# Kernel tuning notes

Hardware: AMD Instinct MI355X
Metric: run time of the kernel (lower is better)

The kernel has to match this reference:

```python
import jax, jax.numpy as jnp
import numpy as np

N = 4096          # nodes (single graph, batch=None)
E = 65536         # edges (avg degree 16)
C = 256           # hidden_channels
L = 3             # num_layers
H = 8             # attention heads
EPS = 1e-5        # batchnorm eps


def setup_inputs() -> dict:
    key = jax.random.key(0)
    ks = iter(jax.random.split(key, 64))
    s = 0.05
    d = {}
    d['x'] = jax.random.normal(next(ks), (N, 1), dtype=jnp.float32)
    d['edge_index'] = jax.random.randint(next(ks), (2, E), 0, N, dtype=jnp.int32)
    # input projection Linear(1, C)
    d['lin1_w'] = jax.random.normal(next(ks), (C, 1), dtype=jnp.float32) * s
    d['lin1_b'] = jnp.zeros((C,), dtype=jnp.float32)
    # GIN MLP: Linear(C,C) -> ReLU -> Linear(C,C), stacked over layers
    d['gin_w1'] = jax.random.normal(next(ks), (L, C, C), dtype=jnp.float32) * s
    d['gin_b1'] = jnp.zeros((L, C), dtype=jnp.float32)
    d['gin_w2'] = jax.random.normal(next(ks), (L, C, C), dtype=jnp.float32) * s
    d['gin_b2'] = jnp.zeros((L, C), dtype=jnp.float32)
    # MultiheadAttention projections
    for nm in ['attn_wq', 'attn_wk', 'attn_wv', 'attn_wo']:
        d[nm] = jax.random.normal(next(ks), (L, C, C), dtype=jnp.float32) * s
    for nm in ['attn_bq', 'attn_bk', 'attn_bv', 'attn_bo']:
        d[nm] = jnp.zeros((L, C), dtype=jnp.float32)
    # three BatchNorms per GPSConv layer
    for nm in ['bn1', 'bn2', 'bn3']:
        d[nm + '_g'] = jnp.ones((L, C), dtype=jnp.float32)
        d[nm + '_b'] = jnp.zeros((L, C), dtype=jnp.float32)
    # GPSConv feedforward: Linear(C, 2C) -> ReLU -> Linear(2C, C)
    d['mlp_w1'] = jax.random.normal(next(ks), (L, 2 * C, C), dtype=jnp.float32) * s
    d['mlp_b1'] = jnp.zeros((L, 2 * C), dtype=jnp.float32)
    d['mlp_w2'] = jax.random.normal(next(ks), (L, C, 2 * C), dtype=jnp.float32) * s
    d['mlp_b2'] = jnp.zeros((L, C), dtype=jnp.float32)
    return d


def _bn(v, g, b):
    # training-mode BatchNorm1d over the node dimension (biased variance)
    m = v.mean(0)
    var = v.var(0)
    return (v - m) * jax.lax.rsqrt(var + EPS) * g + b


def _gps_forward(x, edge_index, lin1_w, lin1_b, gin_w1, gin_b1, gin_w2, gin_b2,
                 attn_wq, attn_bq, attn_wk, attn_bk, attn_wv, attn_bv,
                 attn_wo, attn_bo, bn1_g, bn1_b, bn2_g, bn2_b, bn3_g, bn3_b,
                 mlp_w1, mlp_b1, mlp_w2, mlp_b2):
    h = x @ lin1_w.T + lin1_b                     # [N, C]
    src, dst = edge_index[0], edge_index[1]
    dh = C // H
    scale = 1.0 / jnp.sqrt(jnp.float32(dh))
    for l in range(L):
        xin = h
        # --- GIN branch: gather -> scatter-sum -> MLP ---
        agg = jax.ops.segment_sum(xin[src], dst, num_segments=N)   # [N, C]
        z = xin + agg                                               # eps=0
        z = jax.nn.relu(z @ gin_w1[l].T + gin_b1[l]) @ gin_w2[l].T + gin_b2[l]
        h1 = _bn(z + xin, bn1_g[l], bn1_b[l])
        # --- global multihead attention over all N nodes ---
        q = (xin @ attn_wq[l].T + attn_bq[l]).reshape(N, H, dh)
        k = (xin @ attn_wk[l].T + attn_bk[l]).reshape(N, H, dh)
        v = (xin @ attn_wv[l].T + attn_bv[l]).reshape(N, H, dh)
        scores = jnp.einsum('nhd,mhd->hnm', q, k) * scale           # [H, N, N]
        a = jax.nn.softmax(scores, axis=-1)
        o = jnp.einsum('hnm,mhd->nhd', a, v).reshape(N, C)
        o = o @ attn_wo[l].T + attn_bo[l]
        h2 = _bn(o + xin, bn2_g[l], bn2_b[l])
        # --- combine + feedforward ---
        s = h1 + h2
        m = jax.nn.relu(s @ mlp_w1[l].T + mlp_b1[l]) @ mlp_w2[l].T + mlp_b2[l]
        h = _bn(s + m, bn3_g[l], bn3_b[l])
    return h


def reference(x, edge_index, lin1_w, lin1_b, gin_w1, gin_b1, gin_w2, gin_b2,
              attn_wq, attn_bq, attn_wk, attn_bk, attn_wv, attn_bv,
              attn_wo, attn_bo, bn1_g, bn1_b, bn2_g, bn2_b, bn3_g, bn3_b,
              mlp_w1, mlp_b1, mlp_w2, mlp_b2):
    return _gps_forward(x, edge_index, lin1_w, lin1_b, gin_w1, gin_b1, gin_w2,
                        gin_b2, attn_wq, attn_bq, attn_wk, attn_bk, attn_wv,
                        attn_bv, attn_wo, attn_bo, bn1_g, bn1_b, bn2_g, bn2_b,
                        bn3_g, bn3_b, mlp_w1, mlp_b1, mlp_w2, mlp_b2)
```

## Files before the change

### kernel.cpp

```cpp
#include <hip/hip_runtime.h>

#define NN 4096
#define NE 65536
#define C 256
#define NL 3
#define NH 8
#define DH 32
#define EPS 1e-5f
#define SPLIT 2
#define KT8 (NN/128/SPLIT)
#define ATTN_BLKS ((NN/128)*NH*SPLIT)
#define VS 136

typedef __bf16 bf16x8 __attribute__((ext_vector_type(8)));
typedef __bf16 bf16x4v __attribute__((ext_vector_type(4)));
typedef float f32x4 __attribute__((ext_vector_type(4)));
typedef short bf16x4s __attribute__((ext_vector_type(4)));

#define QSCALE (0.17677669529663687f * 1.4426950408889634f)

#define CC1 (C*C)
#define GS 72

__global__ __launch_bounds__(256) void prep_w(const float* __restrict__ s0,
        const float* __restrict__ s1, const float* __restrict__ s2,
        const float* __restrict__ s3, const float* __restrict__ s4,
        const float* __restrict__ s5, const float* __restrict__ s6,
        const float* __restrict__ s7, __bf16* __restrict__ dst) {
    int g = blockIdx.y;
    int i = (blockIdx.x*256 + threadIdx.x)*4;
    const float* src; int n;
    switch (g) {
        case 0: src=s0; n=3*CC1; break;
        case 1: src=s1; n=3*CC1; break;
        case 2: src=s2; n=3*CC1; break;
        case 3: src=s3; n=3*CC1; break;
        case 4: src=s4; n=3*CC1; break;
        case 5: src=s5; n=3*CC1; break;
        case 6: src=s6; n=6*CC1; break;
        default: src=s7; n=6*CC1; break;
    }
    if (i >= n) return;
    size_t off;
    if (g >= 2 && g <= 4) {
        int l = i >> 16, rem = i & (CC1-1);
        off = (size_t)(6 + 3*l + (g-2))*CC1 + rem;
    } else {
        size_t base = (g==0) ? 0 : (g==1) ? 3*(size_t)CC1 : (g==5) ? 15*(size_t)CC1
                    : (g==6) ? 18*(size_t)CC1 : 24*(size_t)CC1;
        off = base + i;
    }
    float4 t = *(const float4*)(src + i);
    bf16x4v o = {(__bf16)t.x, (__bf16)t.y, (__bf16)t.z, (__bf16)t.w};
    *(bf16x4v*)(dst + off) = o;
}

__global__ __launch_bounds__(256) void lin1_kernel(const float* __restrict__ x,
        const float* __restrict__ w, const float* __restrict__ b,
        __bf16* __restrict__ out) {
    int n = blockIdx.x, c = threadIdx.x;
    out[(size_t)n*C + c] = (__bf16)(x[n]*w[c] + b[c]);
}

__global__ __launch_bounds__(256) void hist_kernel(const int* __restrict__ ei,
        int* __restrict__ cnt) {
    int e = blockIdx.x*256 + threadIdx.x;
    atomicAdd(&cnt[ei[NE + e]], 1);
}

__global__ __launch_bounds__(256) void scan_kernel(const int* __restrict__ cnt,
        int* __restrict__ rowptr, int* __restrict__ cursor) {
    __shared__ int tot[256];
    __shared__ int pre[257];
    int t = threadIdx.x;
    int base = t*16;
    int local[16];
    int s = 0;
    #pragma unroll
    for (int i = 0; i < 16; i++) { local[i] = s; s += cnt[base+i]; }
    tot[t] = s;
    __syncthreads();
    if (t == 0) {
        int acc = 0;
        for (int i = 0; i < 256; i++) { pre[i] = acc; acc += tot[i]; }
        pre[256] = acc;
    }
    __syncthreads();
    int off = pre[t];
    #pragma unroll
    for (int i = 0; i < 16; i++) {
        rowptr[base+i] = off + local[i];
        cursor[base+i] = off + local[i];
    }
    if (t == 0) rowptr[NN] = pre[256];
}

__global__ __launch_bounds__(256) void fill_kernel(const int* __restrict__ ei,
        int* __restrict__ cursor, int* __restrict__ eidsrc) {
    int e = blockIdx.x*256 + threadIdx.x;
    int dst = ei[NE + e], src = ei[e];
    int pos = atomicAdd(&cursor[dst], 1);
    eidsrc[pos] = src;
}

template<int QKV, int BN, int COMB>
__device__ __forceinline__ void gemm_core(int bm, int bn,
        const __bf16* A, const float* A2f, const __bf16* A2b, const __bf16* W,
        const float* b0, const float* b1, const float* b2,
        const __bf16* add1, const __bf16* add2,
        __bf16* out, __bf16* vt, __bf16* ktp, float* stats,
        const float* coefs,
        const float* st1, const float* g1, const float* bb1,
        const float* st2, const float* g2, const float* bb2,
        const float* lsum,
        int K, int Nout, int relu, __bf16* As, __bf16* Ws) {
    int tid = threadIdx.x;
    int wave = tid >> 6, lane = tid & 63;
    int ln = lane & 15, quad = lane >> 4;
    int row = tid >> 2, kseg = (tid & 3) * 16;
    f32x4 acc[4] = {};
    for (int k0 = 0; k0 < K; k0 += 64) {
        __syncthreads();
        {
            bf16x8 a0, a1;
            if constexpr (COMB) {
                int rowg = bm + row;
                int head = (k0 + kseg) >> 5;
                float w[SPLIT];
                float tot = 0.f;
                #pragma unroll
                for (int zz = 0; zz < SPLIT; zz++) {
                    w[zz] = lsum[((size_t)zz*NH + head)*NN + rowg];
                    tot += w[zz];
                }
                float inv = 1.0f / tot;
                float v[16] = {};
                #pragma unroll
                for (int zz = 0; zz < SPLIT; zz++) {
                    const __bf16* p = &A[((size_t)zz*NN + rowg)*C + k0 + kseg];
                    bf16x8 x0 = *(const bf16x8*)p, x1 = *(const bf16x8*)(p + 8);
                    #pragma unroll
                    for (int j = 0; j < 8; j++) {
                        v[j]   += w[zz]*(float)x0[j];
                        v[8+j] += w[zz]*(float)x1[j];
                    }
                }
                #pragma unroll
                for (int j = 0; j < 8; j++) {
                    a0[j] = (__bf16)(v[j]*inv);
                    a1[j] = (__bf16)(v[8+j]*inv);
                }
            } else {
                const __bf16* ap = &A[(size_t)(bm+row)*K + k0 + kseg];
                a0 = *(const bf16x8*)ap;
                a1 = *(const bf16x8*)(ap + 8);
                if constexpr (BN == 1) {
                    const __bf16* p = &A2b[(size_t)(bm+row)*K + k0 + kseg];
                    bf16x8 z0 = *(const bf16x8*)p;
                    bf16x8 z1v = *(const bf16x8*)(p + 8);
                    float sc1[16], sh1[16], sc2[16], sh2[16];
                    #pragma unroll
                    for (int i = 0; i < 4; i++) {
                        *(float4*)&sc1[i*4] = *(const float4*)&coefs[k0 + kseg + i*4];
                        *(float4*)&sh1[i*4] = *(const float4*)&coefs[C + k0 + kseg + i*4];
                        *(float4*)&sc2[i*4] = *(const float4*)&coefs[2*C + k0 + kseg + i*4];
                        *(float4*)&sh2[i*4] = *(const float4*)&coefs[3*C + k0 + kseg + i*4];
                    }
                    #pragma unroll
                    for (int j = 0; j < 8; j++) {
                        a0[j] = (__bf16)((float)a0[j]*sc1[j] + sh1[j]
                                       + (float)z0[j]*sc2[j] + sh2[j]);
                        a1[j] = (__bf16)((float)a1[j]*sc1[8+j] + sh1[8+j]
                                       + (float)z1v[j]*sc2[8+j] + sh2[8+j]);
                    }
                } else if (A2f) {
                    const float* p = &A2f[(size_t)(bm+row)*K + k0 + kseg];
                    float4 t0 = *(const float4*)p;
                    float4 t1 = *(const float4*)(p+4);
                    float4 t2 = *(const float4*)(p+8);
                    float4 t3 = *(const float4*)(p+12);
                    a0[0]=(__bf16)((float)a0[0]+t0.x); a0[1]=(__bf16)((float)a0[1]+t0.y);
                    a0[2]=(__bf16)((float)a0[2]+t0.z); a0[3]=(__bf16)((float)a0[3]+t0.w);
                    a0[4]=(__bf16)((float)a0[4]+t1.x); a0[5]=(__bf16)((float)a0[5]+t1.y);
                    a0[6]=(__bf16)((float)a0[6]+t1.z); a0[7]=(__bf16)((float)a0[7]+t1.w);
                    a1[0]=(__bf16)((float)a1[0]+t2.x); a1[1]=(__bf16)((float)a1[1]+t2.y);
                    a1[2]=(__bf16)((float)a1[2]+t2.z); a1[3]=(__bf16)((float)a1[3]+t2.w);
                    a1[4]=(__bf16)((float)a1[4]+t3.x); a1[5]=(__bf16)((float)a1[5]+t3.y);
                    a1[6]=(__bf16)((float)a1[6]+t3.z); a1[7]=(__bf16)((float)a1[7]+t3.w);
                }
            }
            *(bf16x8*)&As[row*GS + kseg]     = a0;
            *(bf16x8*)&As[row*GS + kseg + 8] = a1;
            const __bf16* wp = &W[(size_t)(bn+row)*K + k0 + kseg];
            *(bf16x8*)&Ws[row*GS + kseg]     = *(const bf16x8*)wp;
            *(bf16x8*)&Ws[row*GS + kseg + 8] = *(const bf16x8*)(wp + 8);
        }
        __syncthreads();
        #pragma unroll
        for (int kt2 = 0; kt2 < 2; kt2++) {
            bf16x8 bfr = *(const bf16x8*)&Ws[(wave*16+ln)*GS + kt2*32 + quad*8];
            #pragma unroll
            for (int i = 0; i < 4; i++) {
                bf16x8 afr = *(const bf16x8*)&As[(i*16+ln)*GS + kt2*32 + quad*8];
                acc[i] = __builtin_amdgcn_mfma_f32_16x16x32_bf16(afr, bfr, acc[i], 0, 0, 0);
            }
        }
    }
    int col = bn + wave*16 + ln;
    if constexpr (QKV) {
        float bsv = col < 256 ? b0[col] : (col < 512 ? b1[col-256] : b2[col-512]);
        if (col < 256) {
            #pragma unroll
            for (int i = 0; i < 4; i++)
                #pragma unroll
                for (int rr = 0; rr < 4; rr++)
                    out[(size_t)(bm + i*16 + quad*4 + rr)*C + col] =
                        (__bf16)((acc[i][rr] + bsv) * (float)QSCALE);
        } else if (col < 512) {
            int hd = (col-256) >> 5, dh = (col-256) & 31;
            #pragma unroll
            for (int i = 0; i < 4; i++)
                #pragma unroll
                for (int rr = 0; rr < 4; rr++)
                    ktp[((size_t)hd*NN + bm + i*16 + quad*4 + rr)*DH + dh] =
                        (__bf16)(acc[i][rr] + bsv);
        } else {
            int vrow = col - 512;
            #pragma unroll
            for (int i = 0; i < 4; i++) {
                bf16x4v pk = {(__bf16)(acc[i][0]+bsv), (__bf16)(acc[i][1]+bsv),
                              (__bf16)(acc[i][2]+bsv), (__bf16)(acc[i][3]+bsv)};
                *(bf16x4v*)&vt[(size_t)vrow*NN + bm + i*16 + quad*4] = pk;
            }
        }
        return;
    }
    float bsv = b0[col];
    float sc1 = 0.f, sh1 = 0.f, sc2 = 0.f, sh2 = 0.f;
    if constexpr (BN == 2) {
        float m1 = st1[col]*(1.f/NN);
        sc1 = rsqrtf(st1[C+col]*(1.f/NN) - m1*m1 + EPS) * g1[col];
        sh1 = bb1[col] - m1*sc1;
        float m2 = st2[col]*(1.f/NN);
        sc2 = rsqrtf(st2[C+col]*(1.f/NN) - m2*m2 + EPS) * g2[col];
        sh2 = bb2[col] - m2*sc2;
    }
    float ssum = 0.f, ssq = 0.f;
    #pragma unroll
    for (int i = 0; i < 4; i++) {
        #pragma unroll
        for (int rr = 0; rr < 4; rr++) {
            int rw = bm + i*16 + quad*4 + rr;
            float vv = acc[i][rr] + bsv;
            if (relu) vv = fmaxf(vv, 0.f);
            size_t idx = (size_t)rw*Nout + col;
            if constexpr (BN == 2) {
                vv += (float)add1[idx]*sc1 + sh1 + (float)add2[idx]*sc2 + sh2;
            } else {
                if (add1) vv += (float)add1[idx];
                if (add2) vv += (float)add2[idx];
            }
            out[idx] = (__bf16)vv;
            ssum += vv; ssq += vv*vv;
        }
    }
    if (stats) {
        ssum += __shfl_xor(ssum, 16); ssum += __shfl_xor(ssum, 32);
        ssq  += __shfl_xor(ssq, 16);  ssq  += __shfl_xor(ssq, 32);
        if (quad == 0) {
            atomicAdd(&stats[col], ssum);
            atomicAdd(&stats[Nout + col], ssq);
        }
    }
}

__device__ __forceinline__ void attn_body(int t, const __bf16* __restrict__ qbuf,
        const __bf16* __restrict__ kt, const __bf16* __restrict__ vt,
        __bf16* __restrict__ opart, float* __restrict__ lsum, __bf16* lds) {
    int head = t & 7, z = t >> 8, qi = (t >> 3) & 31, qb = qi * 128;
    int hb = head * DH;
    int tid = threadIdx.x;
    int wave = tid >> 6, lane = tid & 63;
    int ln = lane & 15, quad = lane >> 4;
    __bf16* Kb0 = lds;
    __bf16* Kb1 = lds + 4608;
    __bf16* Vb0 = lds + 9216;
    __bf16* Vb1 = lds + 9216 + 32*VS;

    bf16x8 qf[2];
    #pragma unroll
    for (int g = 0; g < 2; g++)
        qf[g] = *(const bf16x8*)&qbuf[(size_t)(qb + wave*32 + g*16 + ln)*C + hb + quad*8];

    f32x4 ot[2][2] = {};
    f32x4 la[2] = {};
    const bf16x4s ones = {(short)0x3F80, (short)0x3F80, (short)0x3F80, (short)0x3F80};
    const f32x4 zz = {0.f,0.f,0.f,0.f};

    int srow = tid >> 1, sseg = (tid & 1) * 16;
    int vd = tid >> 3, vseg = (tid & 7) * 16;
    int kt0 = z * KT8;
    const __bf16* kbase = &kt[(size_t)head*NN*DH];
    {
        int i0 = qi & (KT8-1);
        const __bf16* kp = &kbase[(size_t)((kt0+i0)*128 + srow)*DH + sseg];
        *(bf16x8*)&Kb0[srow*36 + sseg]     = *(const bf16x8*)kp;
        *(bf16x8*)&Kb0[srow*36 + sseg + 8] = *(const bf16x8*)(kp + 8);
        const __bf16* vp = &vt[(size_t)(hb + vd)*NN + (kt0+i0)*128 + vseg];
        *(bf16x8*)&Vb0[vd*VS + vseg]     = *(const bf16x8*)vp;
        *(bf16x8*)&Vb0[vd*VS + vseg + 8] = *(const bf16x8*)(vp + 8);
    }
    for (int ii = 0; ii < KT8; ii++) {
        int inext = (ii + 1 + qi) & (KT8-1);
        __bf16* Kc = (ii & 1) ? Kb1 : Kb0;
        __bf16* Kn = (ii & 1) ? Kb0 : Kb1;
        __bf16* Vc = (ii & 1) ? Vb1 : Vb0;
        __bf16* Vn = (ii & 1) ? Vb0 : Vb1;
        __syncthreads();
        bf16x8 nk0, nk1, nv0, nv1;
        bool hasNext = (ii + 1 < KT8);
        if (hasNext) {
            const __bf16* kp = &kbase[(size_t)((kt0+inext)*128 + srow)*DH + sseg];
            nk0 = *(const bf16x8*)kp;
            nk1 = *(const bf16x8*)(kp + 8);
            const __bf16* vp = &vt[(size_t)(hb + vd)*NN + (kt0+inext)*128 + vseg];
            nv0 = *(const bf16x8*)vp;
            nv1 = *(const bf16x8*)(vp + 8);
        }
        bf16x8 kfr[2][2];
        bf16x4s vfr[2][2][2];
        f32x4 stq[2][4];
        kfr[0][0] = *(const bf16x8*)&Kc[((0*16)+ln)*36 + quad*8];
        kfr[0][1] = *(const bf16x8*)&Kc[((1*16)+ln)*36 + quad*8];
        stq[0][0] = __builtin_amdgcn_mfma_f32_16x16x32_bf16(kfr[0][0], qf[0], zz, 0, 0, 0);
        stq[0][1] = __builtin_amdgcn_mfma_f32_16x16x32_bf16(kfr[0][0], qf[1], zz, 0, 0, 0);
        stq[0][2] = __builtin_amdgcn_mfma_f32_16x16x32_bf16(kfr[0][1], qf[0], zz, 0, 0, 0);
        stq[0][3] = __builtin_amdgcn_mfma_f32_16x16x32_bf16(kfr[0][1], qf[1], zz, 0, 0, 0);
        kfr[1][0] = *(const bf16x8*)&Kc[((2*16)+ln)*36 + quad*8];
        kfr[1][1] = *(const bf16x8*)&Kc[((3*16)+ln)*36 + quad*8];
        #pragma unroll
        for (int s = 0; s < 2; s++)
            #pragma unroll
            for (int h = 0; h < 2; h++)
                vfr[0][s][h] = *(const bf16x4s*)&Vc[(h*16+ln)*VS + s*16 + quad*4];
        #pragma unroll
        for (int pr = 0; pr < 4; pr++) {
            const int cur = pr & 1, nxt = cur ^ 1;
            if (pr < 2) {
                kfr[cur][0] = *(const bf16x8*)&Kc[(((pr+2)*2+0)*16+ln)*36 + quad*8];
                kfr[cur][1] = *(const bf16x8*)&Kc[(((pr+2)*2+1)*16+ln)*36 + quad*8];
            }
            if (pr < 3) {
                #pragma unroll
                for (int s = 0; s < 2; s++)
                    #pragma unroll
                    for (int h = 0; h < 2; h++)
                        vfr[nxt][s][h] = *(const bf16x4s*)&Vc[(h*16+ln)*VS + ((pr+1)*2+s)*16 + quad*4];
            }
            if (pr < 3) {
                __builtin_amdgcn_s_setprio(1);
                stq[nxt][0] = __builtin_amdgcn_mfma_f32_16x16x32_bf16(kfr[nxt][0], qf[0], zz, 0, 0, 0);
                stq[nxt][1] = __builtin_amdgcn_mfma_f32_16x16x32_bf16(kfr[nxt][0], qf[1], zz, 0, 0, 0);
                stq[nxt][2] = __builtin_amdgcn_mfma_f32_16x16x32_bf16(kfr[nxt][1], qf[0], zz, 0, 0, 0);
                stq[nxt][3] = __builtin_amdgcn_mfma_f32_16x16x32_bf16(kfr[nxt][1], qf[1], zz, 0, 0, 0);
                __builtin_amdgcn_s_setprio(0);
            }
            union { __bf16 b[4]; bf16x4s s; } pf00, pf01, pf10, pf11;
            #pragma unroll
            for (int rr = 0; rr < 4; rr++) {
                pf00.b[rr] = (__bf16)__builtin_amdgcn_exp2f(stq[cur][0][rr]);
                pf10.b[rr] = (__bf16)__builtin_amdgcn_exp2f(stq[cur][1][rr]);
                pf01.b[rr] = (__bf16)__builtin_amdgcn_exp2f(stq[cur][2][rr]);
                pf11.b[rr] = (__bf16)__builtin_amdgcn_exp2f(stq[cur][3][rr]);
            }
            __builtin_amdgcn_s_setprio(1);
            ot[0][0] = __builtin_amdgcn_mfma_f32_16x16x16bf16_1k(vfr[cur][0][0], pf00.s, ot[0][0], 0, 0, 0);
            ot[0][1] = __builtin_amdgcn_mfma_f32_16x16x16bf16_1k(vfr[cur][0][1], pf00.s, ot[0][1], 0, 0, 0);
            ot[1][0] = __builtin_amdgcn_mfma_f32_16x16x16bf16_1k(vfr[cur][0][0], pf10.s, ot[1][0], 0, 0, 0);
            ot[1][1] = __builtin_amdgcn_mfma_f32_16x16x16bf16_1k(vfr[cur][0][1], pf10.s, ot[1][1], 0, 0, 0);
            la[0]    = __builtin_amdgcn_mfma_f32_16x16x16bf16_1k(ones, pf00.s, la[0], 0, 0, 0);
            la[1]    = __builtin_amdgcn_mfma_f32_16x16x16bf16_1k(ones, pf10.s, la[1], 0, 0, 0);
            ot[0][0] = __builtin_amdgcn_mfma_f32_16x16x16bf16_1k(vfr[cur][1][0], pf01.s, ot[0][0], 0, 0, 0);
            ot[0][1] = __builtin_amdgcn_mfma_f32_16x16x16bf16_1k(vfr[cur][1][1], pf01.s, ot[0][1], 0, 0, 0);
            ot[1][0] = __builtin_amdgcn_mfma_f32_16x16x16bf16_1k(vfr[cur][1][0], pf11.s, ot[1][0], 0, 0, 0);
            ot[1][1] = __builtin_amdgcn_mfma_f32_16x16x16bf16_1k(vfr[cur][1][1], pf11.s, ot[1][1], 0, 0, 0);
            la[0]    = __builtin_amdgcn_mfma_f32_16x16x16bf16_1k(ones, pf01.s, la[0], 0, 0, 0);
            la[1]    = __builtin_amdgcn_mfma_f32_16x16x16bf16_1k(ones, pf11.s, la[1], 0, 0, 0);
            __builtin_amdgcn_s_setprio(0);
        }
        if (hasNext) {
            *(bf16x8*)&Kn[srow*36 + sseg]     = nk0;
            *(bf16x8*)&Kn[srow*36 + sseg + 8] = nk1;
            *(bf16x8*)&Vn[vd*VS + vseg]     = nv0;
            *(bf16x8*)&Vn[vd*VS + vseg + 8] = nv1;
        }
    }
    #pragma unroll
    for (int g = 0; g < 2; g++) {
        float l_ = la[g][0];
        float inv = 1.0f / l_;
        int qrow = qb + wave*32 + g*16 + ln;
        #pragma unroll
        for (int h = 0; h < 2; h++) {
            bf16x4v pk = {(__bf16)(ot[g][h][0]*inv), (__bf16)(ot[g][h][1]*inv),
                          (__bf16)(ot[g][h][2]*inv), (__bf16)(ot[g][h][3]*inv)};
            *(bf16x4v*)&opart[((size_t)z*NN + qrow)*C + hb + h*16 + quad*4] = pk;
        }
        if (quad == 0)
            lsum[((size_t)z*NH + head)*NN + qrow] = l_;
    }
}

__global__ __launch_bounds__(256) void qkv_agg_kernel(const __bf16* __restrict__ Hb,
        const __bf16* __restrict__ Wqkv, const float* __restrict__ bq,
        const float* __restrict__ bk, const float* __restrict__ bv,
        __bf16* __restrict__ qout, __bf16* __restrict__ ktout,
        __bf16* __restrict__ vtout,
        const int* __restrict__ rowptr, const int* __restrict__ eidsrc,
        float* __restrict__ agg) {
    __shared__ __bf16 lds[9216];
    int bx = blockIdx.x;
    if (bx < 768) {
        gemm_core<1,0,0>((bx & 63)*64, (bx >> 6)*64, Hb, nullptr, nullptr, Wqkv,
                bq, bk, bv, nullptr, nullptr, qout, vtout, ktout, nullptr,
                nullptr, nullptr, nullptr, nullptr, nullptr, nullptr, nullptr,
                nullptr, C, 768, 0, lds, lds + 4608);
        return;
    }
    int tid = threadIdx.x;
    int wave = tid >> 6, lane = tid & 63;
    int node = (bx - 768)*4 + wave;
    int beg = rowptr[node], end = rowptr[node+1];
    float s0 = 0.f, s1 = 0.f, s2 = 0.f, s3 = 0.f;
    for (int e = beg; e < end; e++) {
        int src = eidsrc[e];
        bf16x4v hv = *(const bf16x4v*)&Hb[(size_t)src*C + lane*4];
        s0 += (float)hv[0]; s1 += (float)hv[1];
        s2 += (float)hv[2]; s3 += (float)hv[3];
    }
    float4 o = {s0, s1, s2, s3};
    *(float4*)&agg[(size_t)node*C + lane*4] = o;
}

__global__ __launch_bounds__(256, 2) void gin1_attn_kernel(const __bf16* __restrict__ Hb,
        const float* __restrict__ agg, const __bf16* __restrict__ gw1,
        const float* __restrict__ gb1, __bf16* __restrict__ t1,
        const __bf16* __restrict__ qbuf, const __bf16* __restrict__ kt,
        const __bf16* __restrict__ vt,
        __bf16* __restrict__ opart, float* __restrict__ lsum) {
    __shared__ __bf16 lds[17920];
    int bx = blockIdx.x;
    if (bx < 256) {
        gemm_core<0,0,0>((bx >> 2)*64, (bx & 3)*64, Hb, agg, nullptr, gw1,
                gb1, nullptr, nullptr, nullptr, nullptr, t1, nullptr, nullptr,
                nullptr, nullptr, nullptr, nullptr, nullptr, nullptr, nullptr,
                nullptr, nullptr, C, C, 1, lds, lds + 4608);
        return;
    }
    attn_body(bx - 256, qbuf, kt, vt, opart, lsum, lds);
}

__global__ __launch_bounds__(256) void gin2_proj_kernel(const __bf16* __restrict__ t1,
        const __bf16* __restrict__ gw2, const float* __restrict__ gb2,
        const __bf16* __restrict__ Hb, __bf16* __restrict__ z1, float* __restrict__ st1,
        const __bf16* __restrict__ opart, const float* __restrict__ lsum,
        const __bf16* __restrict__ wop, const float* __restrict__ lbo,
        __bf16* __restrict__ z2, float* __restrict__ st2) {
    __shared__ __bf16 lds[9216];
    int bx = blockIdx.x;
    if (bx < 256) {
        gemm_core<0,0,0>((bx >> 2)*64, (bx & 3)*64, t1, nullptr, nullptr, gw2,
                gb2, nullptr, nullptr, Hb, nullptr, z1, nullptr, nullptr, st1,
                nullptr, nullptr, nullptr, nullptr, nullptr, nullptr, nullptr,
                nullptr, C, C, 0, lds, lds + 4608);
        return;
    }
    int t = bx - 256;
    gemm_core<0,0,1>((t >> 2)*64, (t & 3)*64, opart, nullptr, nullptr, wop,
            lbo, nullptr, nullptr, Hb, nullptr, z2, nullptr, nullptr, st2,
            nullptr, nullptr, nullptr, nullptr, nullptr, nullptr, nullptr,
            lsum, C, C, 0, lds, lds + 4608);
}

__global__ __launch_bounds__(256) void ff1_kernel(const __bf16* __restrict__ z1,
        const __bf16* __restrict__ z2, const __bf16* __restrict__ mw1,
        const float* __restrict__ lmb1, __bf16* __restrict__ hidden,
        const float* __restrict__ st1, const float* __restrict__ g1,
        const float* __restrict__ bb1, const float* __restrict__ st2,
        const float* __restrict__ g2, const float* __restrict__ bb2) {
    __shared__ __bf16 lds[9216];
    __shared__ float coefs[4*C];
    int tid = threadIdx.x;
    {
        float m = st1[tid]*(1.f/NN);
        float var = st1[C+tid]*(1.f/NN) - m*m;
        float s = rsqrtf(var + EPS) * g1[tid];
        coefs[tid] = s; coefs[C+tid] = bb1[tid] - m*s;
        m = st2[tid]*(1.f/NN);
        var = st2[C+tid]*(1.f/NN) - m*m;
        s = rsqrtf(var + EPS) * g2[tid];
        coefs[2*C+tid] = s; coefs[3*C+tid] = bb2[tid] - m*s;
    }
    int bx = blockIdx.x;
    gemm_core<0,1,0>((bx >> 3)*64, (bx & 7)*64, z1, nullptr, z2, mw1,
            lmb1, nullptr, nullptr, nullptr, nullptr, hidden, nullptr, nullptr,
            nullptr, coefs, nullptr, nullptr, nullptr, nullptr, nullptr, nullptr,
            nullptr, C, 2*C, 1, lds, lds + 4608);
}

__global__ __launch_bounds__(256) void ff2_kernel(const __bf16* __restrict__ hidden,
        const __bf16* __restrict__ mw2, const float* __restrict__ lmb2,
        const __bf16* __restrict__ z1, const __bf16* __restrict__ z2,
        __bf16* __restrict__ zbuf3, float* __restrict__ st3,
        const float* __restrict__ st1, const float* __restrict__ g1,
        const float* __restrict__ bb1, const float* __restrict__ st2,
        const float* __restrict__ g2, const float* __restrict__ bb2) {
    __shared__ __bf16 lds[9216];
    int bx = blockIdx.x;
    gemm_core<0,2,0>((bx >> 2)*64, (bx & 3)*64, hidden, nullptr, nullptr, mw2,
            lmb2, nullptr, nullptr, z1, z2, zbuf3, nullptr, nullptr, st3,
            nullptr, st1, g1, bb1, st2, g2, bb2,
            nullptr, 2*C, C, 0, lds, lds + 4608);
}

__global__ __launch_bounds__(256) void bn_apply_kernel(const __bf16* __restrict__ z,
        const float* __restrict__ stats, const float* __restrict__ g,
        const float* __restrict__ b, __bf16* __restrict__ outb,
        float* __restrict__ outf) {
    int idx4 = (blockIdx.x*256 + threadIdx.x) * 4;
    int c = idx4 & (C-1);
    bf16x4v zv = *(const bf16x4v*)&z[idx4];
    float4 st = *(const float4*)&stats[c];
    float4 sq = *(const float4*)&stats[C + c];
    float4 gv = *(const float4*)&g[c];
    float4 bv = *(const float4*)&b[c];
    float o[4];
    float m0 = st.x*(1.f/NN), m1 = st.y*(1.f/NN), m2 = st.z*(1.f/NN), m3 = st.w*(1.f/NN);
    o[0] = ((float)zv[0] - m0) * rsqrtf(sq.x*(1.f/NN) - m0*m0 + EPS) * gv.x + bv.x;
    o[1] = ((float)zv[1] - m1) * rsqrtf(sq.y*(1.f/NN) - m1*m1 + EPS) * gv.y + bv.y;
    o[2] = ((float)zv[2] - m2) * rsqrtf(sq.z*(1.f/NN) - m2*m2 + EPS) * gv.z + bv.z;
    o[3] = ((float)zv[3] - m3) * rsqrtf(sq.w*(1.f/NN) - m3*m3 + EPS) * gv.w + bv.w;
    if (outb) {
        bf16x4v ov = {(__bf16)o[0], (__bf16)o[1], (__bf16)o[2], (__bf16)o[3]};
        *(bf16x4v*)&outb[idx4] = ov;
    } else {
        float4 ov = {o[0], o[1], o[2], o[3]};
        *(float4*)&outf[idx4] = ov;
    }
}

extern "C" void kernel_launch(void* const* d_in, const int* in_sizes, int n_in,
                              void* d_out, int out_size, void* d_ws, size_t ws_size,
                              hipStream_t stream) {
    const float* x      = (const float*)d_in[0];
    const int*   ei     = (const int*)d_in[1];
    const float* lin1_w = (const float*)d_in[2];
    const float* lin1_b = (const float*)d_in[3];
    const float* gin_w1 = (const float*)d_in[4];
    const float* gin_b1 = (const float*)d_in[5];
    const float* gin_w2 = (const float*)d_in[6];
    const float* gin_b2 = (const float*)d_in[7];
    const float* wq = (const float*)d_in[8];
    const float* wk = (const float*)d_in[9];
    const float* wv = (const float*)d_in[10];
    const float* wo = (const float*)d_in[11];
    const float* bq = (const float*)d_in[12];
    const float* bk = (const float*)d_in[13];
    const float* bv = (const float*)d_in[14];
    const float* bo = (const float*)d_in[15];
    const float* bn1_g = (const float*)d_in[16];
    const float* bn1_b = (const float*)d_in[17];
    const float* bn2_g = (const float*)d_in[18];
    const float* bn2_b = (const float*)d_in[19];
    const float* bn3_g = (const float*)d_in[20];
    const float* bn3_b = (const float*)d_in[21];
    const float* mw1 = (const float*)d_in[22];
    const float* mb1 = (const float*)d_in[23];
    const float* mw2 = (const float*)d_in[24];
    const float* mb2 = (const float*)d_in[25];

    const size_t MB = 1u << 20;
    char* ws = (char*)d_ws;
    __bf16* Hb      = (__bf16*)(ws);
    __bf16* z1      = (__bf16*)(ws + 2*MB);
    __bf16* zbuf3   = (__bf16*)(ws + 4*MB);
    __bf16* z2      = (__bf16*)(ws + 6*MB);
    __bf16* t1      = (__bf16*)(ws + 8*MB);
    __bf16* Qbuf    = (__bf16*)(ws + 10*MB);
    __bf16* Ktb     = (__bf16*)(ws + 12*MB);
    __bf16* Vt      = (__bf16*)(ws + 14*MB);
    float*  agg     = (float*)(ws + 16*MB);
    __bf16* hiddenb = (__bf16*)(ws + 16*MB);
    __bf16* Opart   = (__bf16*)(ws + 20*MB);
    __bf16* Wb      = (__bf16*)(ws + 28*MB);
    float*  stats   = (float*)(ws + 32*MB);
    int*    cursor  = (int*)(ws + 32*MB + 64*1024);
    int*    rowptr  = (int*)(ws + 32*MB + 96*1024);
    int*    eidsrc  = (int*)(ws + 32*MB + 128*1024);
    float*  lsum    = (float*)(ws + 33*MB);

    dim3 blk(256);

    prep_w<<<dim3(384, 8), blk, 0, stream>>>(gin_w1, gin_w2, wq, wk, wv, wo, mw1, mw2, Wb);
    hipMemsetAsync(stats, 0, 9 * 2 * C * sizeof(float), stream);
    lin1_kernel<<<NN, blk, 0, stream>>>(x, lin1_w, lin1_b, Hb);
    hipMemsetAsync(cursor, 0, NN * sizeof(int), stream);
    hist_kernel<<<NE/256, blk, 0, stream>>>(ei, cursor);
    scan_kernel<<<1, blk, 0, stream>>>(cursor, rowptr, cursor);
    fill_kernel<<<NE/256, blk, 0, stream>>>(ei, cursor, eidsrc);

    for (int l = 0; l < NL; l++) {
        const __bf16* gw1b = Wb + (size_t)l*CC1;
        const __bf16* gw2b = Wb + (size_t)(3+l)*CC1;
        const __bf16* wqkv = Wb + (size_t)(6+3*l)*CC1;
        const __bf16* wop  = Wb + (size_t)(15+l)*CC1;
        const __bf16* mw1p = Wb + (size_t)(18+2*l)*CC1;
        const __bf16* mw2p = Wb + (size_t)(24+2*l)*CC1;
        const float* gb1 = gin_b1 + (size_t)l*C;
        const float* gb2 = gin_b2 + (size_t)l*C;
        const float* lbq = bq + (size_t)l*C;
        const float* lbk = bk + (size_t)l*C;
        const float* lbv = bv + (size_t)l*C;
        const float* lbo = bo + (size_t)l*C;
        const float* lmb1 = mb1 + (size_t)l*2*C;
        const float* lmb2 = mb2 + (size_t)l*C;
        float* st1 = stats + (size_t)l*3*2*C;
        float* st2 = st1 + 2*C;
        float* st3 = st2 + 2*C;
        const float* g1v = bn1_g + (size_t)l*C; const float* b1v = bn1_b + (size_t)l*C;
        const float* g2v = bn2_g + (size_t)l*C; const float* b2v = bn2_b + (size_t)l*C;

        qkv_agg_kernel<<<768 + NN/4, blk, 0, stream>>>(Hb, wqkv, lbq, lbk, lbv,
                Qbuf, Ktb, Vt, rowptr, eidsrc, agg);
        gin1_attn_kernel<<<256 + ATTN_BLKS, blk, 0, stream>>>(Hb, agg,
                gw1b, gb1, t1, Qbuf, Ktb, Vt, Opart, lsum);
        gin2_proj_kernel<<<512, blk, 0, stream>>>(t1, gw2b, gb2, Hb, z1, st1,
                Opart, lsum, wop, lbo, z2, st2);
        ff1_kernel<<<512, blk, 0, stream>>>(z1, z2, mw1p, lmb1, hiddenb,
                st1, g1v, b1v, st2, g2v, b2v);
        ff2_kernel<<<256, blk, 0, stream>>>(hiddenb, mw2p, lmb2, z1, z2,
                zbuf3, st3, st1, g1v, b1v, st2, g2v, b2v);
        if (l == NL-1)
            bn_apply_kernel<<<NN/4, blk, 0, stream>>>(zbuf3, st3,
                    bn3_g + (size_t)l*C, bn3_b + (size_t)l*C, nullptr, (float*)d_out);
        else
            bn_apply_kernel<<<NN/4, blk, 0, stream>>>(zbuf3, st3,
                    bn3_g + (size_t)l*C, bn3_b + (size_t)l*C, Hb, nullptr);
    }
}
```

Measured before the change: 432.9 us.

## Enlarge attention query tile to 256 rows and split keys four ways

Each attention block now covers 256 query rows (64 per wave) instead of 128, and the key range is split four ways instead of two, so the block count stays the same. Each K/V tile staged in LDS is reused by twice as many queries, which cuts LDS traffic and global K/V loads per query. The software-pipelined fragment prefetch and s_setprio hints are replaced by a simpler per-slice loop. This raises register pressure from the doubled accumulators, doubles the partial outputs that must be merged, and may expose LDS latency now that fragments are no longer prefetched.

After: 392.6 us. 1.1x faster.

```diff
diff --git a/kernel.cpp b/kernel.cpp
--- a/kernel.cpp
+++ b/kernel.cpp
@@ -7,9 +7,10 @@
 #define NH 8
 #define DH 32
 #define EPS 1e-5f
-#define SPLIT 2
+#define SPLIT 4
 #define KT8 (NN/128/SPLIT)
-#define ATTN_BLKS ((NN/128)*NH*SPLIT)
+#define QB 256
+#define ATTN_BLKS ((NN/QB)*NH*SPLIT)
 #define VS 136
 
 typedef __bf16 bf16x8 __attribute__((ext_vector_type(8)));
@@ -277,7 +278,8 @@
 __device__ __forceinline__ void attn_body(int t, const __bf16* __restrict__ qbuf,
         const __bf16* __restrict__ kt, const __bf16* __restrict__ vt,
         __bf16* __restrict__ opart, float* __restrict__ lsum, __bf16* lds) {
-    int head = t & 7, z = t >> 8, qi = (t >> 3) & 31, qb = qi * 128;
+    int head = t & 7, qi = (t >> 3) & 15, z = t >> 7;
+    int qb = qi * QB;
     int hb = head * DH;
     int tid = threadIdx.x;
     int wave = tid >> 6, lane = tid & 63;
@@ -287,13 +289,13 @@
     __bf16* Vb0 = lds + 9216;
     __bf16* Vb1 = lds + 9216 + 32*VS;
 
-    bf16x8 qf[2];
+    bf16x8 qf[4];
     #pragma unroll
-    for (int g = 0; g < 2; g++)
-        qf[g] = *(const bf16x8*)&qbuf[(size_t)(qb + wave*32 + g*16 + ln)*C + hb + quad*8];
-
-    f32x4 ot[2][2] = {};
-    f32x4 la[2] = {};
+    for (int g = 0; g < 4; g++)
+        qf[g] = *(const bf16x8*)&qbuf[(size_t)(qb + wave*64 + g*16 + ln)*C + hb + quad*8];
+
+    f32x4 ot[4][2] = {};
+    f32x4 la[4] = {};
     const bf16x4s ones = {(short)0x3F80, (short)0x3F80, (short)0x3F80, (short)0x3F80};
     const f32x4 zz = {0.f,0.f,0.f,0.f};
 
@@ -327,66 +329,39 @@
             nv0 = *(const bf16x8*)vp;
             nv1 = *(const bf16x8*)(vp + 8);
         }
-        bf16x8 kfr[2][2];
-        bf16x4s vfr[2][2][2];
-        f32x4 stq[2][4];
-        kfr[0][0] = *(const bf16x8*)&Kc[((0*16)+ln)*36 + quad*8];
-        kfr[0][1] = *(const bf16x8*)&Kc[((1*16)+ln)*36 + quad*8];
-        stq[0][0] = __builtin_amdgcn_mfma_f32_16x16x32_bf16(kfr[0][0], qf[0], zz, 0, 0, 0);
-        stq[0][1] = __builtin_amdgcn_mfma_f32_16x16x32_bf16(kfr[0][0], qf[1], zz, 0, 0, 0);
-        stq[0][2] = __builtin_amdgcn_mfma_f32_16x16x32_bf16(kfr[0][1], qf[0], zz, 0, 0, 0);
-        stq[0][3] = __builtin_amdgcn_mfma_f32_16x16x32_bf16(kfr[0][1], qf[1], zz, 0, 0, 0);
-        kfr[1][0] = *(const bf16x8*)&Kc[((2*16)+ln)*36 + quad*8];
-        kfr[1][1] = *(const bf16x8*)&Kc[((3*16)+ln)*36 + quad*8];
-        #pragma unroll
-        for (int s = 0; s < 2; s++)
-            #pragma unroll
-            for (int h = 0; h < 2; h++)
-                vfr[0][s][h] = *(const bf16x4s*)&Vc[(h*16+ln)*VS + s*16 + quad*4];
         #pragma unroll
         for (int pr = 0; pr < 4; pr++) {
-            const int cur = pr & 1, nxt = cur ^ 1;
-            if (pr < 2) {
-                kfr[cur][0] = *(const bf16x8*)&Kc[(((pr+2)*2+0)*16+ln)*36 + quad*8];
-                kfr[cur][1] = *(const bf16x8*)&Kc[(((pr+2)*2+1)*16+ln)*36 + quad*8];
+            #pragma unroll
+            for (int s = 0; s < 2; s++) {
+                int ks = pr*2 + s;
+                bf16x8 kf = *(const bf16x8*)&Kc[(ks*16+ln)*36 + quad*8];
+                bf16x4s vf0 = *(const bf16x4s*)&Vc[(0*16+ln)*VS + ks*16 + quad*4];
+                bf16x4s vf1 = *(const bf16x4s*)&Vc[(1*16+ln)*VS + ks*16 + quad*4];
+                f32x4 st0 = __builtin_amdgcn_mfma_f32_16x16x32_bf16(kf, qf[0], zz, 0, 0, 0);
+                f32x4 st1 = __builtin_amdgcn_mfma_f32_16x16x32_bf16(kf, qf[1], zz, 0, 0, 0);
+                f32x4 st2 = __builtin_amdgcn_mfma_f32_16x16x32_bf16(kf, qf[2], zz, 0, 0, 0);
+                f32x4 st3 = __builtin_amdgcn_mfma_f32_16x16x32_bf16(kf, qf[3], zz, 0, 0, 0);
+                union { __bf16 b[4]; bf16x4s s; } pf0, pf1, pf2, pf3;
+                #pragma unroll
+                for (int rr = 0; rr < 4; rr++) {
+                    pf0.b[rr] = (__bf16)__builtin_amdgcn_exp2f(st0[rr]);
+                    pf1.b[rr] = (__bf16)__builtin_amdgcn_exp2f(st1[rr]);
+                    pf2.b[rr] = (__bf16)__builtin_amdgcn_exp2f(st2[rr]);
+                    pf3.b[rr] = (__bf16)__builtin_amdgcn_exp2f(st3[rr]);
+                }
+                ot[0][0] = __builtin_amdgcn_mfma_f32_16x16x16bf16_1k(vf0, pf0.s, ot[0][0], 0, 0, 0);
+                ot[0][1] = __builtin_amdgcn_mfma_f32_16x16x16bf16_1k(vf1, pf0.s, ot[0][1], 0, 0, 0);
+                ot[1][0] = __builtin_amdgcn_mfma_f32_16x16x16bf16_1k(vf0, pf1.s, ot[1][0], 0, 0, 0);
+                ot[1][1] = __builtin_amdgcn_mfma_f32_16x16x16bf16_1k(vf1, pf1.s, ot[1][1], 0, 0, 0);
+                ot[2][0] = __builtin_amdgcn_mfma_f32_16x16x16bf16_1k(vf0, pf2.s, ot[2][0], 0, 0, 0);
+                ot[2][1] = __builtin_amdgcn_mfma_f32_16x16x16bf16_1k(vf1, pf2.s, ot[2][1], 0, 0, 0);
+                ot[3][0] = __builtin_amdgcn_mfma_f32_16x16x16bf16_1k(vf0, pf3.s, ot[3][0], 0, 0, 0);
+                ot[3][1] = __builtin_amdgcn_mfma_f32_16x16x16bf16_1k(vf1, pf3.s, ot[3][1], 0, 0, 0);
+                la[0]    = __builtin_amdgcn_mfma_f32_16x16x16bf16_1k(ones, pf0.s, la[0], 0, 0, 0);
+                la[1]    = __builtin_amdgcn_mfma_f32_16x16x16bf16_1k(ones, pf1.s, la[1], 0, 0, 0);
+                la[2]    = __builtin_amdgcn_mfma_f32_16x16x16bf16_1k(ones, pf2.s, la[2], 0, 0, 0);
+                la[3]    = __builtin_amdgcn_mfma_f32_16x16x16bf16_1k(ones, pf3.s, la[3], 0, 0, 0);
             }
-            if (pr < 3) {
-                #pragma unroll
-                for (int s = 0; s < 2; s++)
-                    #pragma unroll
-                    for (int h = 0; h < 2; h++)
-                        vfr[nxt][s][h] = *(const bf16x4s*)&Vc[(h*16+ln)*VS + ((pr+1)*2+s)*16 + quad*4];
-            }
-            if (pr < 3) {
-                __builtin_amdgcn_s_setprio(1);
-                stq[nxt][0] = __builtin_amdgcn_mfma_f32_16x16x32_bf16(kfr[nxt][0], qf[0], zz, 0, 0, 0);
-                stq[nxt][1] = __builtin_amdgcn_mfma_f32_16x16x32_bf16(kfr[nxt][0], qf[1], zz, 0, 0, 0);
-                stq[nxt][2] = __builtin_amdgcn_mfma_f32_16x16x32_bf16(kfr[nxt][1], qf[0], zz, 0, 0, 0);
-                stq[nxt][3] = __builtin_amdgcn_mfma_f32_16x16x32_bf16(kfr[nxt][1], qf[1], zz, 0, 0, 0);
-                __builtin_amdgcn_s_setprio(0);
-            }
-            union { __bf16 b[4]; bf16x4s s; } pf00, pf01, pf10, pf11;
-            #pragma unroll
-            for (int rr = 0; rr < 4; rr++) {
-                pf00.b[rr] = (__bf16)__builtin_amdgcn_exp2f(stq[cur][0][rr]);
-                pf10.b[rr] = (__bf16)__builtin_amdgcn_exp2f(stq[cur][1][rr]);
-                pf01.b[rr] = (__bf16)__builtin_amdgcn_exp2f(stq[cur][2][rr]);
-                pf11.b[rr] = (__bf16)__builtin_amdgcn_exp2f(stq[cur][3][rr]);
-            }
-            __builtin_amdgcn_s_setprio(1);
-            ot[0][0] = __builtin_amdgcn_mfma_f32_16x16x16bf16_1k(vfr[cur][0][0], pf00.s, ot[0][0], 0, 0, 0);
-            ot[0][1] = __builtin_amdgcn_mfma_f32_16x16x16bf16_1k(vfr[cur][0][1], pf00.s, ot[0][1], 0, 0, 0);
-            ot[1][0] = __builtin_amdgcn_mfma_f32_16x16x16bf16_1k(vfr[cur][0][0], pf10.s, ot[1][0], 0, 0, 0);
-            ot[1][1] = __builtin_amdgcn_mfma_f32_16x16x16bf16_1k(vfr[cur][0][1], pf10.s, ot[1][1], 0, 0, 0);
-            la[0]    = __builtin_amdgcn_mfma_f32_16x16x16bf16_1k(ones, pf00.s, la[0], 0, 0, 0);
-            la[1]    = __builtin_amdgcn_mfma_f32_16x16x16bf16_1k(ones, pf10.s, la[1], 0, 0, 0);
-            ot[0][0] = __builtin_amdgcn_mfma_f32_16x16x16bf16_1k(vfr[cur][1][0], pf01.s, ot[0][0], 0, 0, 0);
-            ot[0][1] = __builtin_amdgcn_mfma_f32_16x16x16bf16_1k(vfr[cur][1][1], pf01.s, ot[0][1], 0, 0, 0);
-            ot[1][0] = __builtin_amdgcn_mfma_f32_16x16x16bf16_1k(vfr[cur][1][0], pf11.s, ot[1][0], 0, 0, 0);
-            ot[1][1] = __builtin_amdgcn_mfma_f32_16x16x16bf16_1k(vfr[cur][1][1], pf11.s, ot[1][1], 0, 0, 0);
-            la[0]    = __builtin_amdgcn_mfma_f32_16x16x16bf16_1k(ones, pf01.s, la[0], 0, 0, 0);
-            la[1]    = __builtin_amdgcn_mfma_f32_16x16x16bf16_1k(ones, pf11.s, la[1], 0, 0, 0);
-            __builtin_amdgcn_s_setprio(0);
         }
         if (hasNext) {
             *(bf16x8*)&Kn[srow*36 + sseg]     = nk0;
@@ -396,10 +371,10 @@
         }
     }
     #pragma unroll
-    for (int g = 0; g < 2; g++) {
+    for (int g = 0; g < 4; g++) {
         float l_ = la[g][0];
         float inv = 1.0f / l_;
-        int qrow = qb + wave*32 + g*16 + ln;
+        int qrow = qb + wave*64 + g*16 + ln;
         #pragma unroll
         for (int h = 0; h < 2; h++) {
             bf16x4v pk = {(__bf16)(ot[g][h][0]*inv), (__bf16)(ot[g][h][1]*inv),
```
